# Optimization experiments

Measured on AMD Instinct MI355X. Metric: run time of the kernel, lower is better.

The kernel has to match this reference:

```python
import jax, jax.numpy as jnp
import numpy as np

F, C, H, W = 16, 256, 64, 64
N, M = 4096, 8192


def setup_inputs() -> dict:
    key = jax.random.key(0)
    k1, k2, k3, k4, k5 = jax.random.split(key, 5)
    proj_mats = jax.random.normal(k1, (F, 3, 3), dtype=jnp.float32)
    feats = jax.random.normal(k2, (F, C, H, W), dtype=jnp.float32)
    feat_img = jax.random.randint(k3, (N, 1), 0, F, dtype=jnp.int32)
    feat_loc = jax.random.uniform(k4, (N, 2), dtype=jnp.float32) * 64.0
    # tracks: [2, M] matched feature pairs, smaller index first (code contract).
    pair = jax.random.randint(k5, (2, M), 0, N, dtype=jnp.int32)
    tracks = jnp.sort(pair, axis=0)
    return {"proj_mats": proj_mats, "feats": feats, "feat_img": feat_img,
            "feat_loc": feat_loc, "tracks": tracks, "n_img": F}


def _association(tracks, n, n_img):
    """Faithful translation of find_3d_point_association +
    associate_3d_point_indices_2_features. The torch code raises a sparse
    symmetric adjacency (with identity diagonal) to the n_img-th power and
    uses only its NONZERO PATTERN. We use binary exponentiation with
    saturation (min(.,1)), which preserves the nonzero pattern exactly
    (all values are non-negative) while keeping values bounded."""
    A = jnp.zeros((n, n), dtype=jnp.float32)
    A = A.at[tracks[0], tracks[1]].set(1.0)
    A = A.at[tracks[1], tracks[0]].set(1.0)
    d = jnp.arange(n)
    A = A.at[d, d].set(1.0)  # identity diagonal, as in the torch code

    # T = pattern(A ** n_img) via binary exponentiation (n_img is a Python int)
    R, P, e = None, A, int(n_img)
    while e:
        if e & 1:
            R = P if R is None else jnp.minimum(R @ P, 1.0)
        e >>= 1
        if e:
            P = jnp.minimum(P @ P, 1.0)
    T = R

    # leading[j] = min{ i : T[i,j] != 0, i <= j }  (diag guarantees j itself)
    rows = d[:, None]
    cand = jnp.where((T > 0) & (rows <= d[None, :]), rows, n)
    leading = cand.min(axis=0)  # [N] int32

    # self-leading features get consecutive 3D-point ids in index order;
    # everyone else inherits the id of its (self-leading) leading feature.
    is_self = leading == d
    point_id = jnp.cumsum(is_self.astype(jnp.int32)) - 1  # rank among self-leading
    association = point_id[leading]
    return association


def reference(proj_mats, feats, feat_img, feat_loc, tracks, n_img):
    n = feat_img.shape[0]
    association = _association(tracks, n, n_img)
    return association
```

## Files before the change

### kernel.cpp

```cpp
#include <hip/hip_runtime.h>

#define NTHREADS 1024
#define MAXN 4096
#define EPT 8
#define NWAVES (NTHREADS / 64)


__device__ __forceinline__ void unite_min(int* p, int u, int v) {
    while (u != v) {
        if (u > v) { int t = u; u = v; v = t; }
        int old = atomicMin(&p[v], u);
        if (old == v) return;
        v = old;
    }
}

__device__ __forceinline__ int find_ro(const int* p, int x) {
    int px = p[x];
    while (px != x) { x = px; px = p[x]; }
    return x;
}

__global__ __launch_bounds__(NTHREADS) void ba_assoc_kernel(
    const int* __restrict__ tracks,
    int* __restrict__ out,
    int N, int M)
{
    const int tid  = threadIdx.x;
    const int lane = tid & 63;
    const int wid  = tid >> 6;

    __shared__ int par[MAXN];
    __shared__ int wsum[NWAVES];

    int eu[EPT], ev[EPT];
#pragma unroll
    for (int k = 0; k < EPT; ++k) {
        int e = tid + k * NTHREADS;
        if (e < M) { eu[k] = tracks[e]; ev[k] = tracks[M + e]; }
        else       { eu[k] = 0;         ev[k] = 0;             }
    }

    for (int i = tid; i < N; i += NTHREADS) par[i] = i;
    __syncthreads();

#pragma unroll
    for (int k = 0; k < EPT; ++k) unite_min(par, eu[k], ev[k]);
    __syncthreads();

    const int base = tid * 4;
#pragma unroll
    for (int r = 0; r < 2; ++r) {
#pragma unroll
        for (int k = 0; k < 4; ++k) {
            int idx = base + k;
            if (idx < N) {
                int p1 = par[idx];
                int p2 = par[p1];
                if (p2 < p1) par[idx] = p2;
            }
        }
        __syncthreads();
    }

    int lead[4], f[4], s = 0;
#pragma unroll
    for (int k = 0; k < 4; ++k) {
        int idx = base + k;
        int r = (idx < N) ? find_ro(par, idx) : 0;
        lead[k] = r;
        int fl = (idx < N && r == idx) ? 1 : 0;
        f[k] = fl;
        s += fl;
    }

    int ps = s;
#pragma unroll
    for (int off = 1; off < 64; off <<= 1) {
        int t = __shfl_up(ps, off, 64);
        if (lane >= off) ps += t;
    }
    if (lane == 63) wsum[wid] = ps;
    __syncthreads();
    int wpre = 0;
    for (int w = 0; w < wid; ++w) wpre += wsum[w];
    int run = wpre + ps - s;

    __syncthreads();
#pragma unroll
    for (int k = 0; k < 4; ++k) {
        int idx = base + k;
        run += f[k];
        if (idx < N) par[idx] = run - 1;
    }
    __syncthreads();

#pragma unroll
    for (int k = 0; k < 4; ++k) {
        int idx = base + k;
        if (idx < N) out[idx] = par[lead[k]];
    }
}

extern "C" void kernel_launch(void* const* d_in, const int* in_sizes, int n_in,
                              void* d_out, int out_size, void* d_ws, size_t ws_size,
                              hipStream_t stream) {
    const int* tracks = (const int*)d_in[4];
    int* out = (int*)d_out;
    const int N = in_sizes[2];
    const int M = in_sizes[4] / 2;
    ba_assoc_kernel<<<1, NTHREADS, 0, stream>>>(tracks, out, N, M);
}
```

Before: 17.06 us.

## Halve threads, fuse pointer-jumping into find, drop barriers, vectorize output stores

Drops to 512 threads, each handling 16 edges and 8 nodes. The two separate pointer-jumping passes, each followed by a barrier, become a single path-halving step done inline before each find. One redundant barrier before the scan write-back is removed. The wave-prefix loop is unrolled, and output is written with int4 stores. Bounds checks are gone, so the kernel now assumes N equals 512*8 and is 16-byte aligned. Fewer threads also means more serial union-find work per thread.

```diff
diff --git a/kernel.cpp b/kernel.cpp
--- a/kernel.cpp
+++ b/kernel.cpp
@@ -1,8 +1,9 @@
 #include <hip/hip_runtime.h>
 
-#define NTHREADS 1024
+#define NTHREADS 512
 #define MAXN 4096
-#define EPT 8
+#define EPT 16
+#define NPT 8
 #define NWAVES (NTHREADS / 64)
 
 
@@ -48,28 +49,17 @@
     for (int k = 0; k < EPT; ++k) unite_min(par, eu[k], ev[k]);
     __syncthreads();
 
-    const int base = tid * 4;
+    const int base = tid * NPT;
+    int lead[NPT], f[NPT], s = 0;
 #pragma unroll
-    for (int r = 0; r < 2; ++r) {
-#pragma unroll
-        for (int k = 0; k < 4; ++k) {
-            int idx = base + k;
-            if (idx < N) {
-                int p1 = par[idx];
-                int p2 = par[p1];
-                if (p2 < p1) par[idx] = p2;
-            }
-        }
-        __syncthreads();
-    }
-
-    int lead[4], f[4], s = 0;
-#pragma unroll
-    for (int k = 0; k < 4; ++k) {
+    for (int k = 0; k < NPT; ++k) {
         int idx = base + k;
-        int r = (idx < N) ? find_ro(par, idx) : 0;
+        int p1 = par[idx];
+        int p2 = par[p1];
+        if (p2 < p1) { par[idx] = p2; p1 = p2; }
+        int r = find_ro(par, p1);
         lead[k] = r;
-        int fl = (idx < N && r == idx) ? 1 : 0;
+        int fl = (r == idx) ? 1 : 0;
         f[k] = fl;
         s += fl;
     }
@@ -83,23 +73,22 @@
     if (lane == 63) wsum[wid] = ps;
     __syncthreads();
     int wpre = 0;
-    for (int w = 0; w < wid; ++w) wpre += wsum[w];
+#pragma unroll
+    for (int w = 0; w < NWAVES - 1; ++w) if (w < wid) wpre += wsum[w];
     int run = wpre + ps - s;
 
-    __syncthreads();
 #pragma unroll
-    for (int k = 0; k < 4; ++k) {
-        int idx = base + k;
+    for (int k = 0; k < NPT; ++k) {
         run += f[k];
-        if (idx < N) par[idx] = run - 1;
+        par[base + k] = run - 1;
     }
     __syncthreads();
 
+    int res[NPT];
 #pragma unroll
-    for (int k = 0; k < 4; ++k) {
-        int idx = base + k;
-        if (idx < N) out[idx] = par[lead[k]];
-    }
+    for (int k = 0; k < NPT; ++k) res[k] = par[lead[k]];
+    ((int4*)(out + base))[0] = make_int4(res[0], res[1], res[2], res[3]);
+    ((int4*)(out + base))[1] = make_int4(res[4], res[5], res[6], res[7]);
 }
 
 extern "C" void kernel_launch(void* const* d_in, const int* in_sizes, int n_in,
```

After: 21.34 us. +25.0%, slower.
